# Kernel optimization log

Measured on AMD Instinct MI355X. Metric: run time of the kernel, lower is better.

## Reference

```python
import jax, jax.numpy as jnp
import numpy as np

PS = 16          # patch size == conv kernel == stride
EPS = 1e-5       # BatchNorm eps (torch default)


def setup_inputs() -> dict:
    key = jax.random.key(0)
    ks = jax.random.split(key, 12)
    B, Cin, H = 64, 3, 256
    D, Dm = 3, 768                      # private_depth, hidden_dim
    P = (H // PS) ** 2                  # num_patches = 256

    x = jax.random.normal(ks[0], (B, Cin, H, H), jnp.float32)
    # patch-embed conv: weight [O, I, kh, kw], bias [O]
    conv0_w = jax.random.normal(ks[1], (Dm, Cin, PS, PS), jnp.float32) * 0.02
    conv0_b = jax.random.normal(ks[2], (Dm,), jnp.float32) * 0.02
    # depth x (1x1 conv + BN): stacked params
    w1 = jax.random.normal(ks[3], (D, Dm, Dm), jnp.float32) * 0.02   # [O, I]
    b1 = jax.random.normal(ks[4], (D, Dm), jnp.float32) * 0.02
    gamma = jnp.ones((D, Dm), jnp.float32)
    beta = jnp.zeros((D, Dm), jnp.float32)
    # positional embedding [1, P, Dm]
    pos_emb = jax.random.normal(ks[5], (1, P, Dm), jnp.float32)
    # mixer Linear [out, in] + bias
    mixer_w = jax.random.normal(ks[6], (Dm, Dm), jnp.float32) * 0.02
    mixer_b = jax.random.normal(ks[7], (Dm,), jnp.float32) * 0.02
    # per-sample random permutation of the P patches (replaces randperm loop)
    perm = jax.vmap(lambda k: jax.random.permutation(k, P))(
        jax.random.split(ks[8], B)).astype(jnp.int32)

    return {"x": x, "conv0_w": conv0_w, "conv0_b": conv0_b, "w1": w1,
            "b1": b1, "gamma": gamma, "beta": beta, "pos_emb": pos_emb,
            "mixer_w": mixer_w, "mixer_b": mixer_b, "perm": perm}


def reference(x, conv0_w, conv0_b, w1, b1, gamma, beta, pos_emb,
              mixer_w, mixer_b, perm):
    B, Cin, H, W = x.shape
    hp, wp = H // PS, W // PS
    Dm = conv0_w.shape[0]

    # non-overlapping patch conv == reshape + matmul
    # x -> [B, hp*wp, Cin*PS*PS] with (c, kh, kw) flattening matching conv weight
    patches = x.reshape(B, Cin, hp, PS, wp, PS).transpose(0, 2, 4, 1, 3, 5)
    patches = patches.reshape(B, hp * wp, Cin * PS * PS)
    h = jax.nn.relu(patches @ conv0_w.reshape(Dm, -1).T + conv0_b)  # [B, P, Dm]

    # private_depth x (1x1 conv -> BN (batch stats, no running stats) -> ReLU)
    for d in range(w1.shape[0]):
        h = h @ w1[d].T + b1[d]
        mu = h.mean(axis=(0, 1))                      # per-channel over (B, H*W)
        var = ((h - mu) ** 2).mean(axis=(0, 1))       # biased variance
        h = (h - mu) * jax.lax.rsqrt(var + EPS) * gamma[d] + beta[d]
        h = jax.nn.relu(h)

    # pos embedding + mixer (ReLU -> Linear)
    h = h + pos_emb
    h = jax.nn.relu(h) @ mixer_w.T + mixer_b          # [B, P, Dm]

    # per-sample pixel shuffle: shuffled[i, j] = h[i, perm[i, j]]
    out = jnp.take_along_axis(h, perm[:, :, None].astype(jnp.int32), axis=1)
    return out
```

## Files before the change

kernel.cpp:

```cpp
#include <hip/hip_runtime.h>
#include <hip/hip_bf16.h>
#include <stdint.h>

#define M_TOT 16384
#define DM 768
#define BM 256
#define BN 192
#define NKT3 12
#define QOFF (128 * DM)

typedef __attribute__((ext_vector_type(4))) float f32x4;
typedef __attribute__((ext_vector_type(8))) short short8;
typedef __attribute__((ext_vector_type(4))) unsigned short ushort4v;

__device__ __forceinline__ unsigned short f2bf(float f) {
    union { float f; unsigned u; } v; v.f = f;
    unsigned r = v.u + 0x7fffu + ((v.u >> 16) & 1u);
    return (unsigned short)(r >> 16);
}
__device__ __forceinline__ float bf2f(unsigned short h) {
    union { unsigned u; float f; } v; v.u = ((unsigned)h) << 16;
    return v.f;
}

__device__ __forceinline__ void gload_lds16(const unsigned short* g, unsigned short* l) {
    __builtin_amdgcn_global_load_lds(
        (const __attribute__((address_space(1))) void*)g,
        (__attribute__((address_space(3))) void*)l, 16, 0, 0);
}

__global__ __launch_bounds__(256)
void prep(const float* __restrict__ cw, const float* __restrict__ w1,
          const float* __restrict__ mw, const int* __restrict__ perm,
          unsigned short* __restrict__ wA, unsigned short* __restrict__ wD,
          unsigned short* __restrict__ wM, int* __restrict__ invp)
{
    int b = blockIdx.x;
    if (b < 2880) {
        int i = b * 256 + threadIdx.x;
        const float* src; unsigned short* dst; int off;
        if (i < 147456)              { src = cw; dst = wA; off = i; }
        else if (i < 147456+442368)  { src = w1; dst = wD; off = i - 147456; }
        else                         { src = mw; dst = wM; off = i - 589824; }
        f32x4 v = ((const f32x4*)src)[off];
        ushort4v o;
        o.x = f2bf(v.x); o.y = f2bf(v.y); o.z = f2bf(v.z); o.w = f2bf(v.w);
        ((ushort4v*)dst)[off] = o;
    } else {
        int i = (b - 2880) * 256 + threadIdx.x;
        int bb = i >> 8;
        invp[(bb << 8) + perm[i]] = i & 255;
    }
}

__global__ __launch_bounds__(256)
void im2col(const float* __restrict__ x, unsigned short* __restrict__ patches)
{
    int t = blockIdx.x * 256 + threadIdx.x;
    int bp = t / 192;
    int q  = t - bp * 192;
    int c   = q >> 6;
    int kh  = (q >> 2) & 15;
    int kw0 = (q & 3) << 2;
    int b = bp >> 8, p = bp & 255;
    int ph = p >> 4, pw = p & 15;
    const float* src = x + ((((size_t)b * 3 + c) * 256 + ph * 16 + kh) * 256 + pw * 16 + kw0);
    f32x4 v = *(const f32x4*)src;
    ushort4v o;
    o.x = f2bf(v.x); o.y = f2bf(v.y); o.z = f2bf(v.z); o.w = f2bf(v.w);
    *(ushort4v*)(patches + (size_t)bp * DM + (q << 2)) = o;
}

#define VM4  asm volatile("s_waitcnt vmcnt(4)" ::: "memory");
#define VM0  asm volatile("s_waitcnt vmcnt(0)" ::: "memory");
#define BARR asm volatile("s_barrier" ::: "memory");
#define NOVM

#define DO_PHASE(AB, BB, MH, KS, LOADB, VMC, ...)                                \
  {                                                                              \
    if (LOADB) {                                                                 \
      _Pragma("unroll")                                                          \
      for (int j = 0; j < 3; ++j)                                                \
        breg[j] = *(const short8*)((const char*)Bb[BB] +                         \
                  (wc * 48 + j * 16 + frow) * 128 + (((KS) * 64 + fq16) ^ rswz));\
    }                                                                            \
    short8 af[4];                                                                \
    _Pragma("unroll")                                                            \
    for (int i = 0; i < 4; ++i)                                                  \
      af[i] = *(const short8*)((const char*)Aa[AB] +                             \
              (wr * 128 + (MH) * 64 + i * 16 + frow) * 128 +                     \
              (((KS) * 64 + fq16) ^ rswz));                                      \
    __VA_ARGS__;                                                                 \
    __builtin_amdgcn_s_setprio(1);                                               \
    _Pragma("unroll")                                                            \
    for (int i = 0; i < 4; ++i)                                                  \
      _Pragma("unroll")                                                          \
      for (int j = 0; j < 3; ++j)                                                \
        acc[(MH) * 4 + i][j] = __builtin_amdgcn_mfma_f32_16x16x32_bf16(          \
            af[i], breg[j], acc[(MH) * 4 + i][j], 0, 0, 0);                      \
    __builtin_amdgcn_s_setprio(0);                                               \
    VMC                                                                          \
    BARR                                                                         \
  }

template<int EPI>
__global__ __launch_bounds__(512, 2)
void gemm8p(const unsigned short* __restrict__ A,
            const unsigned short* __restrict__ Bw,
            const float* __restrict__ bias,
            void* __restrict__ outp,
            const int* __restrict__ invp,
            float* __restrict__ bnpart)
{
    __shared__ unsigned short Aa[3][BM * 64];
    __shared__ unsigned short Bb[2][BN * 64];

    const int tid  = threadIdx.x;
    const int w    = tid >> 6;
    const int lane = tid & 63;
    const int wr = w >> 2, wc = w & 3;

    int bid = blockIdx.x;
    int nb  = (bid & 7) * 32 + (bid >> 3);
    const int tileM = nb >> 2, tileN = nb & 3;
    const int m0 = tileM * BM, n0 = tileN * BN;

    const int sRow = lane >> 3;
    const int swzc = ((lane & 7) * 16) ^ ((sRow & 7) << 4);
    const unsigned short* gA0 = A  + (size_t)(m0 + w * 32 + sRow) * DM + (swzc >> 1);
    const unsigned short* gB0 = Bw + (size_t)(n0 + w * 24 + sRow) * DM + (swzc >> 1);

    auto STAGE_A = [&](int buf, int kt) {
        #pragma unroll
        for (int j = 0; j < 4; ++j)
            gload_lds16(gA0 + (size_t)j * 8 * DM + kt * 64,
                        &Aa[buf][(w * 32 + j * 8) * 64]);
    };
    auto STAGE_B = [&](int buf, int kt) {
        #pragma unroll
        for (int j = 0; j < 3; ++j)
            gload_lds16(gB0 + (size_t)j * 8 * DM + kt * 64,
                        &Bb[buf][(w * 24 + j * 8) * 64]);
    };

    const int frow = lane & 15;
    const int fq16 = (lane >> 4) * 16;
    const int rswz = (lane & 7) << 4;

    f32x4 acc[8][3] = {};
    short8 breg[3];

    STAGE_A(0, 0);
    STAGE_B(0, 0);
    STAGE_A(1, 1);
    VM4
    BARR

    #pragma unroll
    for (int kt = 0; kt < NKT3; ++kt) {
        const int ab = kt % 3, bb = kt & 1;
        DO_PHASE(ab, bb, 0, 0, 1, NOVM, if (kt < 11) STAGE_B((kt + 1) & 1, kt + 1))
        DO_PHASE(ab, bb, 1, 0, 0, NOVM, if (kt < 10) STAGE_A((kt + 2) % 3, kt + 2))
        DO_PHASE(ab, bb, 0, 1, 1, NOVM, )
        if (kt < 10)       { DO_PHASE(ab, bb, 1, 1, 0, VM4, ) }
        else if (kt == 10) { DO_PHASE(ab, bb, 1, 1, 0, VM0, ) }
        else               { DO_PHASE(ab, bb, 1, 1, 0, NOVM, ) }
    }

    const int crow = (lane >> 4) * 4;
    const int ccol = lane & 15;
    const int nbase = n0 + wc * 48;

    float bv[3];
    #pragma unroll
    for (int j = 0; j < 3; ++j) bv[j] = bias[nbase + j * 16 + ccol];

    if (EPI == 2) {
        float* O = (float*)outp;
        #pragma unroll
        for (int mi = 0; mi < 8; ++mi) {
            #pragma unroll
            for (int r = 0; r < 4; ++r) {
                int m = m0 + wr * 128 + mi * 16 + crow + r;
                int mo = (m & ~255) | invp[m];
                float* orow = O + (size_t)mo * DM + nbase + ccol;
                #pragma unroll
                for (int j = 0; j < 3; ++j)
                    orow[j * 16] = acc[mi][j][r] + bv[j];
            }
        }
    } else {
        unsigned short* O = (unsigned short*)outp;
        #pragma unroll
        for (int mi = 0; mi < 8; ++mi) {
            #pragma unroll
            for (int r = 0; r < 4; ++r) {
                int m = m0 + wr * 128 + mi * 16 + crow + r;
                unsigned short* orow = O + (size_t)m * DM + nbase + ccol;
                #pragma unroll
                for (int j = 0; j < 3; ++j) {
                    float v = acc[mi][j][r] + bv[j];
                    if (EPI == 0) v = fmaxf(v, 0.0f);
                    orow[j * 16] = f2bf(v);
                }
            }
        }
    }

    if (EPI == 1) {
        #pragma unroll
        for (int j = 0; j < 3; ++j) {
            float s = 0.f, q = 0.f;
            #pragma unroll
            for (int mi = 0; mi < 8; ++mi)
                #pragma unroll
                for (int r = 0; r < 4; ++r) {
                    float v = acc[mi][j][r] + bv[j];
                    s += v; q += v * v;
                }
            s += __shfl_xor(s, 16); s += __shfl_xor(s, 32);
            q += __shfl_xor(q, 16); q += __shfl_xor(q, 32);
            if (lane < 16) {
                int c = nbase + j * 16 + lane;
                bnpart[(tileM * 2 + wr) * DM + c] = s;
                bnpart[QOFF + (tileM * 2 + wr) * DM + c] = q;
            }
        }
    }
}

__global__ void bn_stats(const float* __restrict__ part, const float* __restrict__ gamma,
                         const float* __restrict__ beta, float* __restrict__ ss)
{
    int c = blockIdx.x * 256 + threadIdx.x;
    float s = 0.f, q = 0.f;
    #pragma unroll 4
    for (int b = 0; b < 128; ++b) {
        s += part[b * DM + c];
        q += part[QOFF + b * DM + c];
    }
    float mu  = s * (1.0f / 16384.0f);
    float var = q * (1.0f / 16384.0f) - mu * mu;
    float scale = rsqrtf(var + 1e-5f) * gamma[c];
    ss[c] = scale;
    ss[DM + c] = beta[c] - mu * scale;
}

template<int POS>
__global__ __launch_bounds__(256)
void bn_apply(const unsigned short* __restrict__ hin, const float* __restrict__ ss,
              const float* __restrict__ pos, unsigned short* __restrict__ hout)
{
    __shared__ float sc[DM], sh[DM];
    const int t = threadIdx.x;
    #pragma unroll
    for (int i = 0; i < 3; ++i) {
        sc[t + i * 256] = ss[t + i * 256];
        sh[t + i * 256] = ss[DM + t + i * 256];
    }
    __syncthreads();

    int g = blockIdx.x * 256 + t;
    int row = g / 96;
    int c0 = (g - row * 96) * 8;
    const short8 v = *(const short8*)(hin + (size_t)row * DM + c0);
    short8 o;
    #pragma unroll
    for (int e = 0; e < 8; ++e) {
        float xv = bf2f((unsigned short)v[e]);
        float y = fmaxf(xv * sc[c0 + e] + sh[c0 + e], 0.0f);
        if (POS) y = fmaxf(y + pos[(row & 255) * DM + c0 + e], 0.0f);
        o[e] = (short)f2bf(y);
    }
    *(short8*)(hout + (size_t)row * DM + c0) = o;
}

extern "C" void kernel_launch(void* const* d_in, const int* in_sizes, int n_in,
                              void* d_out, int out_size, void* d_ws, size_t ws_size,
                              hipStream_t stream)
{
    (void)in_sizes; (void)n_in; (void)out_size; (void)ws_size;

    const float* x       = (const float*)d_in[0];
    const float* conv0_w = (const float*)d_in[1];
    const float* conv0_b = (const float*)d_in[2];
    const float* w1      = (const float*)d_in[3];
    const float* b1      = (const float*)d_in[4];
    const float* gamma   = (const float*)d_in[5];
    const float* beta    = (const float*)d_in[6];
    const float* pos     = (const float*)d_in[7];
    const float* mixer_w = (const float*)d_in[8];
    const float* mixer_b = (const float*)d_in[9];
    const int*   perm    = (const int*)d_in[10];

    unsigned short* actA = (unsigned short*)d_ws;
    unsigned short* actB = actA + (size_t)M_TOT * DM;
    unsigned short* wA   = actB + (size_t)M_TOT * DM;
    unsigned short* wD   = wA + DM * DM;
    unsigned short* wM   = wD + 3 * DM * DM;
    float* bnpart = (float*)(wM + DM * DM);
    float* ss     = bnpart + 2 * 128 * DM;
    int*   invp   = (int*)(ss + 2 * DM);

    prep<<<2944, 256, 0, stream>>>(conv0_w, w1, mixer_w, perm, wA, wD, wM, invp);
    im2col<<<12288, 256, 0, stream>>>(x, actA);

    gemm8p<0><<<256, 512, 0, stream>>>(actA, wA, conv0_b, actB, nullptr, nullptr);

    for (int d = 0; d < 3; ++d) {
        gemm8p<1><<<256, 512, 0, stream>>>(actB, wD + (size_t)d * DM * DM, b1 + d * DM,
                                           actA, nullptr, bnpart);
        bn_stats<<<3, 256, 0, stream>>>(bnpart, gamma + d * DM, beta + d * DM, ss);
        if (d < 2) bn_apply<0><<<6144, 256, 0, stream>>>(actA, ss, pos, actB);
        else       bn_apply<1><<<6144, 256, 0, stream>>>(actA, ss, pos, actB);
    }

    gemm8p<2><<<256, 512, 0, stream>>>(actB, wM, mixer_b, d_out, invp, nullptr);
}
```

Baseline: 228.7 us.

## Fuse BatchNorm statistics and apply into GEMM epilogue via grid-wide barrier

Each depth GEMM now writes its per-channel partial sums in a channel-major layout. All blocks then sync through an atomic counter spin barrier, and each block reduces the stats for its own 192 columns into LDS. Scale, shift, ReLU and the optional positional add are applied directly to the accumulators before writing bf16. This removes the separate bn_stats and bn_apply launches and a full read and write of the activation tensor per layer. In exchange it relies on all 256 blocks being co-resident and writes the output in place over the GEMM input, which is only safe because the barrier follows the main loop.

```diff
diff --git a/kernel.cpp b/kernel.cpp
--- a/kernel.cpp
+++ b/kernel.cpp
@@ -33,7 +33,8 @@
 void prep(const float* __restrict__ cw, const float* __restrict__ w1,
           const float* __restrict__ mw, const int* __restrict__ perm,
           unsigned short* __restrict__ wA, unsigned short* __restrict__ wD,
-          unsigned short* __restrict__ wM, int* __restrict__ invp)
+          unsigned short* __restrict__ wM, int* __restrict__ invp,
+          unsigned int* __restrict__ cnt)
 {
     int b = blockIdx.x;
     if (b < 2880) {
@@ -46,10 +47,12 @@
         ushort4v o;
         o.x = f2bf(v.x); o.y = f2bf(v.y); o.z = f2bf(v.z); o.w = f2bf(v.w);
         ((ushort4v*)dst)[off] = o;
-    } else {
+    } else if (b < 2944) {
         int i = (b - 2880) * 256 + threadIdx.x;
         int bb = i >> 8;
         invp[(bb << 8) + perm[i]] = i & 255;
+    } else {
+        if (threadIdx.x < 3) cnt[threadIdx.x] = 0u;
     }
 }
 
@@ -103,14 +106,18 @@
     BARR                                                                         \
   }
 
-template<int EPI>
+template<int EPI, int POS>
 __global__ __launch_bounds__(512, 2)
 void gemm8p(const unsigned short* __restrict__ A,
             const unsigned short* __restrict__ Bw,
             const float* __restrict__ bias,
             void* __restrict__ outp,
             const int* __restrict__ invp,
-            float* __restrict__ bnpart)
+            float* __restrict__ bnpart,
+            const float* __restrict__ gamma,
+            const float* __restrict__ beta,
+            const float* __restrict__ pos,
+            unsigned int* __restrict__ cnt)
 {
     __shared__ unsigned short Aa[3][BM * 64];
     __shared__ unsigned short Bb[2][BN * 64];
@@ -175,6 +182,21 @@
     #pragma unroll
     for (int j = 0; j < 3; ++j) bv[j] = bias[nbase + j * 16 + ccol];
 
+    if (EPI == 0) {
+        unsigned short* O = (unsigned short*)outp;
+        #pragma unroll
+        for (int mi = 0; mi < 8; ++mi) {
+            #pragma unroll
+            for (int r = 0; r < 4; ++r) {
+                int m = m0 + wr * 128 + mi * 16 + crow + r;
+                unsigned short* orow = O + (size_t)m * DM + nbase + ccol;
+                #pragma unroll
+                for (int j = 0; j < 3; ++j)
+                    orow[j * 16] = f2bf(fmaxf(acc[mi][j][r] + bv[j], 0.0f));
+            }
+        }
+    }
+
     if (EPI == 2) {
         float* O = (float*)outp;
         #pragma unroll
@@ -187,22 +209,6 @@
                 #pragma unroll
                 for (int j = 0; j < 3; ++j)
                     orow[j * 16] = acc[mi][j][r] + bv[j];
-            }
-        }
-    } else {
-        unsigned short* O = (unsigned short*)outp;
-        #pragma unroll
-        for (int mi = 0; mi < 8; ++mi) {
-            #pragma unroll
-            for (int r = 0; r < 4; ++r) {
-                int m = m0 + wr * 128 + mi * 16 + crow + r;
-                unsigned short* orow = O + (size_t)m * DM + nbase + ccol;
-                #pragma unroll
-                for (int j = 0; j < 3; ++j) {
-                    float v = acc[mi][j][r] + bv[j];
-                    if (EPI == 0) v = fmaxf(v, 0.0f);
-                    orow[j * 16] = f2bf(v);
-                }
             }
         }
     }
@@ -221,58 +227,56 @@
             s += __shfl_xor(s, 16); s += __shfl_xor(s, 32);
             q += __shfl_xor(q, 16); q += __shfl_xor(q, 32);
             if (lane < 16) {
-                int c = nbase + j * 16 + lane;
-                bnpart[(tileM * 2 + wr) * DM + c] = s;
-                bnpart[QOFF + (tileM * 2 + wr) * DM + c] = q;
+                int c  = nbase + j * 16 + lane;
+                int ri = tileM * 2 + wr;
+                bnpart[(size_t)c * 128 + ri]        = s;
+                bnpart[QOFF + (size_t)c * 128 + ri] = q;
             }
         }
-    }
-}
-
-__global__ void bn_stats(const float* __restrict__ part, const float* __restrict__ gamma,
-                         const float* __restrict__ beta, float* __restrict__ ss)
-{
-    int c = blockIdx.x * 256 + threadIdx.x;
-    float s = 0.f, q = 0.f;
-    #pragma unroll 4
-    for (int b = 0; b < 128; ++b) {
-        s += part[b * DM + c];
-        q += part[QOFF + b * DM + c];
-    }
-    float mu  = s * (1.0f / 16384.0f);
-    float var = q * (1.0f / 16384.0f) - mu * mu;
-    float scale = rsqrtf(var + 1e-5f) * gamma[c];
-    ss[c] = scale;
-    ss[DM + c] = beta[c] - mu * scale;
-}
-
-template<int POS>
-__global__ __launch_bounds__(256)
-void bn_apply(const unsigned short* __restrict__ hin, const float* __restrict__ ss,
-              const float* __restrict__ pos, unsigned short* __restrict__ hout)
-{
-    __shared__ float sc[DM], sh[DM];
-    const int t = threadIdx.x;
-    #pragma unroll
-    for (int i = 0; i < 3; ++i) {
-        sc[t + i * 256] = ss[t + i * 256];
-        sh[t + i * 256] = ss[DM + t + i * 256];
-    }
-    __syncthreads();
-
-    int g = blockIdx.x * 256 + t;
-    int row = g / 96;
-    int c0 = (g - row * 96) * 8;
-    const short8 v = *(const short8*)(hin + (size_t)row * DM + c0);
-    short8 o;
-    #pragma unroll
-    for (int e = 0; e < 8; ++e) {
-        float xv = bf2f((unsigned short)v[e]);
-        float y = fmaxf(xv * sc[c0 + e] + sh[c0 + e], 0.0f);
-        if (POS) y = fmaxf(y + pos[(row & 255) * DM + c0 + e], 0.0f);
-        o[e] = (short)f2bf(y);
-    }
-    *(short8*)(hout + (size_t)row * DM + c0) = o;
+
+        __threadfence();
+        __syncthreads();
+        if (tid == 0) {
+            __hip_atomic_fetch_add(cnt, 1u, __ATOMIC_ACQ_REL, __HIP_MEMORY_SCOPE_AGENT);
+            while (__hip_atomic_load(cnt, __ATOMIC_ACQUIRE, __HIP_MEMORY_SCOPE_AGENT) < 256u) {}
+        }
+        __syncthreads();
+        __threadfence();
+
+        float* scl = (float*)&Aa[0][0];
+        float* shf = scl + 192;
+        if (tid < 192) {
+            int c = n0 + tid;
+            const float* ps = bnpart + (size_t)c * 128;
+            const float* pq = bnpart + QOFF + (size_t)c * 128;
+            float s = 0.f, q = 0.f;
+            #pragma unroll 8
+            for (int i = 0; i < 128; ++i) { s += ps[i]; q += pq[i]; }
+            float mu  = s * (1.0f / 16384.0f);
+            float var = q * (1.0f / 16384.0f) - mu * mu;
+            float sc_ = rsqrtf(var + 1e-5f) * gamma[c];
+            scl[tid] = sc_;
+            shf[tid] = beta[c] - mu * sc_;
+        }
+        __syncthreads();
+
+        unsigned short* O = (unsigned short*)outp;
+        #pragma unroll
+        for (int mi = 0; mi < 8; ++mi) {
+            #pragma unroll
+            for (int r = 0; r < 4; ++r) {
+                int m = m0 + wr * 128 + mi * 16 + crow + r;
+                unsigned short* orow = O + (size_t)m * DM + nbase + ccol;
+                #pragma unroll
+                for (int j = 0; j < 3; ++j) {
+                    int ci = wc * 48 + j * 16 + ccol;
+                    float y = fmaxf(scl[ci] * (acc[mi][j][r] + bv[j]) + shf[ci], 0.0f);
+                    if (POS) y = fmaxf(y + pos[(m & 255) * DM + n0 + ci], 0.0f);
+                    orow[j * 16] = f2bf(y);
+                }
+            }
+        }
+    }
 }
 
 extern "C" void kernel_launch(void* const* d_in, const int* in_sizes, int n_in,
@@ -299,21 +303,25 @@
     unsigned short* wD   = wA + DM * DM;
     unsigned short* wM   = wD + 3 * DM * DM;
     float* bnpart = (float*)(wM + DM * DM);
-    float* ss     = bnpart + 2 * 128 * DM;
-    int*   invp   = (int*)(ss + 2 * DM);
-
-    prep<<<2944, 256, 0, stream>>>(conv0_w, w1, mixer_w, perm, wA, wD, wM, invp);
+    unsigned int* cnts = (unsigned int*)(bnpart + 2 * 128 * DM);
+    int*   invp   = (int*)(cnts + 4);
+
+    prep<<<2945, 256, 0, stream>>>(conv0_w, w1, mixer_w, perm, wA, wD, wM, invp, cnts);
     im2col<<<12288, 256, 0, stream>>>(x, actA);
 
-    gemm8p<0><<<256, 512, 0, stream>>>(actA, wA, conv0_b, actB, nullptr, nullptr);
-
-    for (int d = 0; d < 3; ++d) {
-        gemm8p<1><<<256, 512, 0, stream>>>(actB, wD + (size_t)d * DM * DM, b1 + d * DM,
-                                           actA, nullptr, bnpart);
-        bn_stats<<<3, 256, 0, stream>>>(bnpart, gamma + d * DM, beta + d * DM, ss);
-        if (d < 2) bn_apply<0><<<6144, 256, 0, stream>>>(actA, ss, pos, actB);
-        else       bn_apply<1><<<6144, 256, 0, stream>>>(actA, ss, pos, actB);
-    }
-
-    gemm8p<2><<<256, 512, 0, stream>>>(actB, wM, mixer_b, d_out, invp, nullptr);
-}
+    gemm8p<0, 0><<<256, 512, 0, stream>>>(actA, wA, conv0_b, actB, nullptr,
+                                          nullptr, nullptr, nullptr, nullptr, nullptr);
+
+    gemm8p<1, 0><<<256, 512, 0, stream>>>(actB, wD + 0 * (size_t)DM * DM, b1 + 0 * DM, actB,
+                                          nullptr, bnpart, gamma + 0 * DM, beta + 0 * DM,
+                                          pos, cnts + 0);
+    gemm8p<1, 0><<<256, 512, 0, stream>>>(actB, wD + 1 * (size_t)DM * DM, b1 + 1 * DM, actB,
+                                          nullptr, bnpart, gamma + 1 * DM, beta + 1 * DM,
+                                          pos, cnts + 1);
+    gemm8p<1, 1><<<256, 512, 0, stream>>>(actB, wD + 2 * (size_t)DM * DM, b1 + 2 * DM, actB,
+                                          nullptr, bnpart, gamma + 2 * DM, beta + 2 * DM,
+                                          pos, cnts + 2);
+
+    gemm8p<2, 0><<<256, 512, 0, stream>>>(actB, wM, mixer_b, d_out, invp,
+                                          nullptr, nullptr, nullptr, nullptr, nullptr);
+}
```

Measured after the change: 468.5 us. 105% more time.

## Fuse BatchNorm apply and pos-embed into next GEMM's A-operand load

Applied to the files above, without the earlier changes.

Removes the standalone bn_apply kernels. The following GEMM now loads raw bf16 activations into registers, applies the BN scale/shift, ReLU and optional pos-embedding, then writes the result to swizzled LDS. This drops one full read and write pass over the 16384x768 activation per layer, at the cost of a register-staged A pipeline with explicit waits that may weaken latency hiding in the GEMM mainloop. The BN partial-sum layout is also transposed so bn_stats reads contiguous per-channel data.

```diff
diff --git a/kernel.cpp b/kernel.cpp
--- a/kernel.cpp
+++ b/kernel.cpp
@@ -11,6 +11,7 @@
 
 typedef __attribute__((ext_vector_type(4))) float f32x4;
 typedef __attribute__((ext_vector_type(8))) short short8;
+typedef __attribute__((ext_vector_type(8))) unsigned short ushort8;
 typedef __attribute__((ext_vector_type(4))) unsigned short ushort4v;
 
 __device__ __forceinline__ unsigned short f2bf(float f) {
@@ -73,24 +74,24 @@
 
 #define VM4  asm volatile("s_waitcnt vmcnt(4)" ::: "memory");
 #define VM0  asm volatile("s_waitcnt vmcnt(0)" ::: "memory");
+#define LGKM0 asm volatile("s_waitcnt lgkmcnt(0)" ::: "memory");
 #define BARR asm volatile("s_barrier" ::: "memory");
-#define NOVM
-
-#define DO_PHASE(AB, BB, MH, KS, LOADB, VMC, ...)                                \
+
+#define PH(AB, BB, MH, KS, LOADB, PRE, POST)                                     \
   {                                                                              \
     if (LOADB) {                                                                 \
       _Pragma("unroll")                                                          \
       for (int j = 0; j < 3; ++j)                                                \
-        breg[j] = *(const short8*)((const char*)Bb[BB] +                         \
+        breg[j] = *(const short8*)((const char*)Bb + (size_t)(BB) * (BN*64*2) +  \
                   (wc * 48 + j * 16 + frow) * 128 + (((KS) * 64 + fq16) ^ rswz));\
     }                                                                            \
     short8 af[4];                                                                \
     _Pragma("unroll")                                                            \
     for (int i = 0; i < 4; ++i)                                                  \
-      af[i] = *(const short8*)((const char*)Aa[AB] +                             \
+      af[i] = *(const short8*)((const char*)Aa + (size_t)(AB) * (BM*64*2) +      \
               (wr * 128 + (MH) * 64 + i * 16 + frow) * 128 +                     \
               (((KS) * 64 + fq16) ^ rswz));                                      \
-    __VA_ARGS__;                                                                 \
+    PRE;                                                                         \
     __builtin_amdgcn_s_setprio(1);                                               \
     _Pragma("unroll")                                                            \
     for (int i = 0; i < 4; ++i)                                                  \
@@ -99,18 +100,20 @@
         acc[(MH) * 4 + i][j] = __builtin_amdgcn_mfma_f32_16x16x32_bf16(          \
             af[i], breg[j], acc[(MH) * 4 + i][j], 0, 0, 0);                      \
     __builtin_amdgcn_s_setprio(0);                                               \
-    VMC                                                                          \
+    POST;                                                                        \
     BARR                                                                         \
   }
 
-template<int EPI>
+template<int EPI, int BNA>
 __global__ __launch_bounds__(512, 2)
 void gemm8p(const unsigned short* __restrict__ A,
             const unsigned short* __restrict__ Bw,
             const float* __restrict__ bias,
             void* __restrict__ outp,
             const int* __restrict__ invp,
-            float* __restrict__ bnpart)
+            float* __restrict__ bnpart,
+            const float* __restrict__ ssA,
+            const float* __restrict__ pos)
 {
     __shared__ unsigned short Aa[3][BM * 64];
     __shared__ unsigned short Bb[2][BN * 64];
@@ -143,6 +146,49 @@
                         &Bb[buf][(w * 24 + j * 8) * 64]);
     };
 
+    const int rRow0 = w * 32 + (lane >> 3);
+    const unsigned short* gAr = A + (size_t)(m0 + rRow0) * DM + (lane & 7) * 8;
+    const int wrswz = (lane >> 3) << 4;
+    ushort8 aldr[4];
+
+    auto ALOAD = [&](int t) {
+        #pragma unroll
+        for (int j = 0; j < 4; ++j)
+            aldr[j] = *(const ushort8*)(gAr + (size_t)j * 8 * DM + t * 64);
+    };
+    auto XFORM = [&](int t, int tb) {
+        const int k0 = t * 64 + (lane & 7) * 8;
+        f32x4 sa = *(const f32x4*)(ssA + k0);
+        f32x4 sb = *(const f32x4*)(ssA + k0 + 4);
+        f32x4 ha = *(const f32x4*)(ssA + DM + k0);
+        f32x4 hb = *(const f32x4*)(ssA + DM + k0 + 4);
+        #pragma unroll
+        for (int j = 0; j < 4; ++j) {
+            int row = rRow0 + j * 8;
+            f32x4 pa, pb;
+            if (BNA == 2) {
+                pa = *(const f32x4*)(pos + row * DM + k0);
+                pb = *(const f32x4*)(pos + row * DM + k0 + 4);
+            }
+            ushort8 u = aldr[j];
+            ushort8 o;
+            #pragma unroll
+            for (int e = 0; e < 8; ++e) {
+                float f = bf2f(u[e]);
+                float sc = (e < 4) ? sa[e] : sb[e - 4];
+                float sh = (e < 4) ? ha[e] : hb[e - 4];
+                float y = fmaxf(fmaf(sc, f, sh), 0.0f);
+                if (BNA == 2) {
+                    float pv = (e < 4) ? pa[e] : pb[e - 4];
+                    y = fmaxf(y + pv, 0.0f);
+                }
+                o[e] = f2bf(y);
+            }
+            *(ushort8*)((char*)Aa + (size_t)tb * (BM*64*2) + row * 128 +
+                        (((lane & 7) * 16) ^ wrswz)) = o;
+        }
+    };
+
     const int frow = lane & 15;
     const int fq16 = (lane >> 4) * 16;
     const int rswz = (lane & 7) << 4;
@@ -150,21 +196,44 @@
     f32x4 acc[8][3] = {};
     short8 breg[3];
 
-    STAGE_A(0, 0);
-    STAGE_B(0, 0);
-    STAGE_A(1, 1);
-    VM4
-    BARR
-
-    #pragma unroll
-    for (int kt = 0; kt < NKT3; ++kt) {
-        const int ab = kt % 3, bb = kt & 1;
-        DO_PHASE(ab, bb, 0, 0, 1, NOVM, if (kt < 11) STAGE_B((kt + 1) & 1, kt + 1))
-        DO_PHASE(ab, bb, 1, 0, 0, NOVM, if (kt < 10) STAGE_A((kt + 2) % 3, kt + 2))
-        DO_PHASE(ab, bb, 0, 1, 1, NOVM, )
-        if (kt < 10)       { DO_PHASE(ab, bb, 1, 1, 0, VM4, ) }
-        else if (kt == 10) { DO_PHASE(ab, bb, 1, 1, 0, VM0, ) }
-        else               { DO_PHASE(ab, bb, 1, 1, 0, NOVM, ) }
+    if (BNA == 0) {
+        STAGE_A(0, 0);
+        STAGE_B(0, 0);
+        STAGE_A(1, 1);
+        VM4
+        BARR
+    } else {
+        ALOAD(0); XFORM(0, 0);
+        ALOAD(1); XFORM(1, 1);
+        STAGE_B(0, 0);
+        VM0
+        LGKM0
+        BARR
+    }
+
+    if (BNA == 0) {
+        #pragma unroll
+        for (int kt = 0; kt < NKT3; ++kt) {
+            const int ab = kt % 3, bb = kt & 1;
+            PH(ab, bb, 0, 0, 1, { if (kt < 11) STAGE_B((kt + 1) & 1, kt + 1); }, {})
+            PH(ab, bb, 1, 0, 0, { if (kt < 10) STAGE_A((kt + 2) % 3, kt + 2); }, {})
+            PH(ab, bb, 0, 1, 1, {}, {})
+            if (kt < 10)       { PH(ab, bb, 1, 1, 0, {}, { VM4 }) }
+            else if (kt == 10) { PH(ab, bb, 1, 1, 0, {}, { VM0 }) }
+            else               { PH(ab, bb, 1, 1, 0, {}, {}) }
+        }
+    } else {
+        #pragma unroll 3
+        for (int kt = 0; kt < NKT3; ++kt) {
+            const int ab = kt % 3, bb = kt & 1;
+            const int ab1 = (ab == 2) ? 0 : ab + 1;
+            PH(ab, bb, 0, 0, 1, { if (kt < 11) STAGE_B((kt + 1) & 1, kt + 1); }, {})
+            PH(ab, bb, 1, 0, 0, { if (kt >= 1 && kt < 11) XFORM(kt + 1, ab1); },
+                                { if (kt >= 1 && kt < 11) LGKM0 })
+            PH(ab, bb, 0, 1, 1, {}, {})
+            PH(ab, bb, 1, 1, 0, {}, { if (kt < 11) VM0
+                                      if (kt < 10) ALOAD(kt + 2); })
+        }
     }
 
     const int crow = (lane >> 4) * 4;
@@ -174,6 +243,21 @@
     float bv[3];
     #pragma unroll
     for (int j = 0; j < 3; ++j) bv[j] = bias[nbase + j * 16 + ccol];
+
+    if (EPI == 0) {
+        unsigned short* O = (unsigned short*)outp;
+        #pragma unroll
+        for (int mi = 0; mi < 8; ++mi) {
+            #pragma unroll
+            for (int r = 0; r < 4; ++r) {
+                int m = m0 + wr * 128 + mi * 16 + crow + r;
+                unsigned short* orow = O + (size_t)m * DM + nbase + ccol;
+                #pragma unroll
+                for (int j = 0; j < 3; ++j)
+                    orow[j * 16] = f2bf(fmaxf(acc[mi][j][r] + bv[j], 0.0f));
+            }
+        }
+    }
 
     if (EPI == 2) {
         float* O = (float*)outp;
@@ -189,7 +273,9 @@
                     orow[j * 16] = acc[mi][j][r] + bv[j];
             }
         }
-    } else {
+    }
+
+    if (EPI == 1) {
         unsigned short* O = (unsigned short*)outp;
         #pragma unroll
         for (int mi = 0; mi < 8; ++mi) {
@@ -198,16 +284,10 @@
                 int m = m0 + wr * 128 + mi * 16 + crow + r;
                 unsigned short* orow = O + (size_t)m * DM + nbase + ccol;
                 #pragma unroll
-                for (int j = 0; j < 3; ++j) {
-                    float v = acc[mi][j][r] + bv[j];
-                    if (EPI == 0) v = fmaxf(v, 0.0f);
-                    orow[j * 16] = f2bf(v);
-                }
-            }
-        }
-    }
-
-    if (EPI == 1) {
+                for (int j = 0; j < 3; ++j)
+                    orow[j * 16] = f2bf(acc[mi][j][r] + bv[j]);
+            }
+        }
         #pragma unroll
         for (int j = 0; j < 3; ++j) {
             float s = 0.f, q = 0.f;
@@ -221,9 +301,10 @@
             s += __shfl_xor(s, 16); s += __shfl_xor(s, 32);
             q += __shfl_xor(q, 16); q += __shfl_xor(q, 32);
             if (lane < 16) {
-                int c = nbase + j * 16 + lane;
-                bnpart[(tileM * 2 + wr) * DM + c] = s;
-                bnpart[QOFF + (tileM * 2 + wr) * DM + c] = q;
+                int c  = nbase + j * 16 + lane;
+                int ri = tileM * 2 + wr;
+                bnpart[(size_t)c * 128 + ri]        = s;
+                bnpart[QOFF + (size_t)c * 128 + ri] = q;
             }
         }
     }
@@ -233,46 +314,16 @@
                          const float* __restrict__ beta, float* __restrict__ ss)
 {
     int c = blockIdx.x * 256 + threadIdx.x;
+    const float* ps = part + (size_t)c * 128;
+    const float* pq = part + QOFF + (size_t)c * 128;
     float s = 0.f, q = 0.f;
-    #pragma unroll 4
-    for (int b = 0; b < 128; ++b) {
-        s += part[b * DM + c];
-        q += part[QOFF + b * DM + c];
-    }
+    #pragma unroll 8
+    for (int i = 0; i < 128; ++i) { s += ps[i]; q += pq[i]; }
     float mu  = s * (1.0f / 16384.0f);
     float var = q * (1.0f / 16384.0f) - mu * mu;
     float scale = rsqrtf(var + 1e-5f) * gamma[c];
     ss[c] = scale;
     ss[DM + c] = beta[c] - mu * scale;
-}
-
-template<int POS>
-__global__ __launch_bounds__(256)
-void bn_apply(const unsigned short* __restrict__ hin, const float* __restrict__ ss,
-              const float* __restrict__ pos, unsigned short* __restrict__ hout)
-{
-    __shared__ float sc[DM], sh[DM];
-    const int t = threadIdx.x;
-    #pragma unroll
-    for (int i = 0; i < 3; ++i) {
-        sc[t + i * 256] = ss[t + i * 256];
-        sh[t + i * 256] = ss[DM + t + i * 256];
-    }
-    __syncthreads();
-
-    int g = blockIdx.x * 256 + t;
-    int row = g / 96;
-    int c0 = (g - row * 96) * 8;
-    const short8 v = *(const short8*)(hin + (size_t)row * DM + c0);
-    short8 o;
-    #pragma unroll
-    for (int e = 0; e < 8; ++e) {
-        float xv = bf2f((unsigned short)v[e]);
-        float y = fmaxf(xv * sc[c0 + e] + sh[c0 + e], 0.0f);
-        if (POS) y = fmaxf(y + pos[(row & 255) * DM + c0 + e], 0.0f);
-        o[e] = (short)f2bf(y);
-    }
-    *(short8*)(hout + (size_t)row * DM + c0) = o;
 }
 
 extern "C" void kernel_launch(void* const* d_in, const int* in_sizes, int n_in,
@@ -305,15 +356,17 @@
     prep<<<2944, 256, 0, stream>>>(conv0_w, w1, mixer_w, perm, wA, wD, wM, invp);
     im2col<<<12288, 256, 0, stream>>>(x, actA);
 
-    gemm8p<0><<<256, 512, 0, stream>>>(actA, wA, conv0_b, actB, nullptr, nullptr);
-
-    for (int d = 0; d < 3; ++d) {
-        gemm8p<1><<<256, 512, 0, stream>>>(actB, wD + (size_t)d * DM * DM, b1 + d * DM,
-                                           actA, nullptr, bnpart);
-        bn_stats<<<3, 256, 0, stream>>>(bnpart, gamma + d * DM, beta + d * DM, ss);
-        if (d < 2) bn_apply<0><<<6144, 256, 0, stream>>>(actA, ss, pos, actB);
-        else       bn_apply<1><<<6144, 256, 0, stream>>>(actA, ss, pos, actB);
-    }
-
-    gemm8p<2><<<256, 512, 0, stream>>>(actB, wM, mixer_b, d_out, invp, nullptr);
-}
+    gemm8p<0, 0><<<256, 512, 0, stream>>>(actA, wA, conv0_b, actB, nullptr,
+                                          nullptr, nullptr, nullptr);
+    gemm8p<1, 0><<<256, 512, 0, stream>>>(actB, wD + 0 * (size_t)DM * DM, b1 + 0 * DM,
+                                          actA, nullptr, bnpart, nullptr, nullptr);
+    bn_stats<<<3, 256, 0, stream>>>(bnpart, gamma + 0 * DM, beta + 0 * DM, ss);
+    gemm8p<1, 1><<<256, 512, 0, stream>>>(actA, wD + 1 * (size_t)DM * DM, b1 + 1 * DM,
+                                          actB, nullptr, bnpart, ss, nullptr);
+    bn_stats<<<3, 256, 0, stream>>>(bnpart, gamma + 1 * DM, beta + 1 * DM, ss);
+    gemm8p<1, 1><<<256, 512, 0, stream>>>(actB, wD + 2 * (size_t)DM * DM, b1 + 2 * DM,
+                                          actA, nullptr, bnpart, ss, nullptr);
+    bn_stats<<<3, 256, 0, stream>>>(bnpart, gamma + 2 * DM, beta + 2 * DM, ss);
+    gemm8p<2, 2><<<256, 512, 0, stream>>>(actA, wM, mixer_b, d_out, invp,
+                                          nullptr, ss, pos);
+}
```

Measured after the change: 212.0 us. -7.3%, faster.
